# Kernel optimization log

Hardware: AMD Instinct MI355X
Metric: run time of the kernel (lower is better)

The kernel has to match this reference:

```python
import jax, jax.numpy as jnp
import numpy as np

B, T, H, U = 32, 2048, 512, 32

def _glorot(key, shape):
    fan_in, fan_out = shape[0], shape[1]
    limit = np.sqrt(6.0 / (fan_in + fan_out))
    return jax.random.uniform(key, shape, jnp.float32, -limit, limit)

def setup_inputs() -> dict:
    key = jax.random.key(0)
    ks = jax.random.split(key, 6)
    return {
        "x": jax.random.normal(ks[0], (B, T, H), jnp.float32),
        "t": jax.random.normal(ks[1], (B, T, H), jnp.float32),
        "kernel_x": _glorot(ks[2], (H, U)),
        "kernel_t": _glorot(ks[3], (H, U)),
        "kernel_a": _glorot(ks[4], (U, H)),
        "bias_x": jnp.zeros((U,), jnp.float32),
        "bias_t": jnp.zeros((U,), jnp.float32),
        "lambd": _glorot(ks[5], (T, 1)),
    }

def reference(x, t, kernel_x, kernel_t, kernel_a, bias_x, bias_t, lambd):
    # gamma, beta: [B, T, U]
    gamma = jnp.tanh(jnp.einsum('bth,hu->btu', x, kernel_x) + bias_x)
    beta = jnp.tanh(jnp.einsum('bth,hu->btu', t, kernel_t) + bias_t)
    # per-timespan convex combination; lambd [T,1] broadcasts over units
    delta = lambd * gamma + (1.0 - lambd) * beta
    # scores [B, T, H]; softmax over the timespan axis (-2)
    scores = jnp.einsum('btu,uh->bth', delta, kernel_a)
    alpha = jax.nn.softmax(scores, axis=-2)
    return alpha
```

## Files before the change

### kernel.cpp

```cpp
#include <hip/hip_runtime.h>
#include <cmath>

#define Hdim 512
#define Udim 32
#define Bdim 32
#define Tdim 2048
#define RM   64
#define KC   32
#define LDX  36
#define NU   8
#define CH   128

__global__ __launch_bounds__(256, 4) void k1_gemm_act(
    const float* __restrict__ x, const float* __restrict__ tin,
    const float* __restrict__ kx, const float* __restrict__ kt,
    const float* __restrict__ bx, const float* __restrict__ bt,
    const float* __restrict__ lambd, float* __restrict__ delta)
{
    __shared__ float xs[RM * LDX];
    __shared__ float ts[RM * LDX];

    const int tid  = threadIdx.x;
    const int lane = tid & 63;
    const int u0   = __builtin_amdgcn_readfirstlane((tid >> 6) * NU);
    const int row0 = blockIdx.x * RM;

    const int srow = tid >> 3;
    const int sf4  = tid & 7;

    const float4* xg = (const float4*)x;
    const float4* tg = (const float4*)tin;

    float4 px[2], pt[2];
    float accx[NU], acct[NU];
#pragma unroll
    for (int uu = 0; uu < NU; ++uu) { accx[uu] = 0.f; acct[uu] = 0.f; }

#pragma unroll
    for (int l = 0; l < 2; ++l) {
        const size_t r = (size_t)(row0 + srow + 32 * l);
        px[l] = xg[r * (Hdim / 4) + sf4];
        pt[l] = tg[r * (Hdim / 4) + sf4];
    }

#pragma unroll 1
    for (int c = 0; c < Hdim / KC; ++c) {
        __syncthreads();
#pragma unroll
        for (int l = 0; l < 2; ++l) {
            *(float4*)&xs[(srow + 32 * l) * LDX + sf4 * 4] = px[l];
            *(float4*)&ts[(srow + 32 * l) * LDX + sf4 * 4] = pt[l];
        }
        __syncthreads();

        if (c + 1 < Hdim / KC) {
#pragma unroll
            for (int l = 0; l < 2; ++l) {
                const size_t r = (size_t)(row0 + srow + 32 * l);
                px[l] = xg[r * (Hdim / 4) + (c + 1) * (KC / 4) + sf4];
                pt[l] = tg[r * (Hdim / 4) + (c + 1) * (KC / 4) + sf4];
            }
        }

#pragma unroll
        for (int q = 0; q < KC / 4; ++q) {
            float4 av = *(const float4*)&xs[lane * LDX + 4 * q];
            float4 bv = *(const float4*)&ts[lane * LDX + 4 * q];
            float a4[4] = { av.x, av.y, av.z, av.w };
            float b4[4] = { bv.x, bv.y, bv.z, bv.w };
            const float* wxp = kx + (size_t)(c * KC + 4 * q) * Udim + u0;
            const float* wtp = kt + (size_t)(c * KC + 4 * q) * Udim + u0;
#pragma unroll
            for (int kk = 0; kk < 4; ++kk)
#pragma unroll
                for (int uu = 0; uu < NU; ++uu) {
                    accx[uu] = fmaf(a4[kk], wxp[kk * Udim + uu], accx[uu]);
                    acct[uu] = fmaf(b4[kk], wtp[kk * Udim + uu], acct[uu]);
                }
        }
    }

    const int grow = row0 + lane;
    const float lam = lambd[grow & (Tdim - 1)];
    float o[NU];
#pragma unroll
    for (int uu = 0; uu < NU; ++uu) {
        float g  = tanhf(accx[uu] + bx[u0 + uu]);
        float be = tanhf(acct[uu] + bt[u0 + uu]);
        o[uu] = lam * g + (1.0f - lam) * be;
    }
    float* dp = delta + (size_t)grow * Udim + u0;
    *(float4*)&dp[0] = make_float4(o[0], o[1], o[2], o[3]);
    *(float4*)&dp[4] = make_float4(o[4], o[5], o[6], o[7]);
}

__global__ __launch_bounds__(1024, 2) void k2_softmax(
    const float* __restrict__ delta, const float* __restrict__ ka_g,
    float* __restrict__ alpha)
{
    __shared__ float dsm[2][CH * Udim];
    __shared__ float ms[16][64];
    __shared__ float ls[16][64];

    const int tid = threadIdx.x;
    const int tx  = tid & 63;
    const int ty  = tid >> 6;
    const int b   = blockIdx.x & 31;
    const int ht  = blockIdx.x >> 5;
    const int h   = ht * 64 + tx;

    float ka[Udim];
#pragma unroll
    for (int u = 0; u < Udim; ++u) ka[u] = ka_g[u * Hdim + h];

    const float4* dsrc = (const float4*)(delta + (size_t)b * Tdim * Udim);

    ((float4*)dsm[0])[tid] = dsrc[tid];

    float m = -1e30f, l = 0.f;
#pragma unroll 1
    for (int c = 0; c < Tdim / CH; ++c) {
        __syncthreads();
        const float* cur = dsm[c & 1];
        if (c + 1 < Tdim / CH)
            ((float4*)dsm[(c + 1) & 1])[tid] = dsrc[(size_t)(c + 1) * (CH * Udim / 4) + tid];
#pragma unroll
        for (int i = 0; i < CH / 16; ++i) {
            const int r = ty + 16 * i;
            const float4* dp = (const float4*)(cur + r * Udim);
            float4 q[8];
#pragma unroll
            for (int j = 0; j < 8; ++j) q[j] = dp[j];
            float s0 = 0.f, s1 = 0.f, s2 = 0.f, s3 = 0.f;
#pragma unroll
            for (int j = 0; j < 8; ++j) {
                s0 = fmaf(q[j].x, ka[4 * j],     s0);
                s1 = fmaf(q[j].y, ka[4 * j + 1], s1);
                s2 = fmaf(q[j].z, ka[4 * j + 2], s2);
                s3 = fmaf(q[j].w, ka[4 * j + 3], s3);
            }
            const float s = (s0 + s1) + (s2 + s3);
            const float mn = fmaxf(m, s);
            l = l * __expf(m - mn) + __expf(s - mn);
            m = mn;
        }
    }

    ms[ty][tx] = m;
    ls[ty][tx] = l;
    __syncthreads();
    float M = -1e30f;
#pragma unroll
    for (int w = 0; w < 16; ++w) M = fmaxf(M, ms[w][tx]);
    float L = 0.f;
#pragma unroll
    for (int w = 0; w < 16; ++w) L += ls[w][tx] * __expf(ms[w][tx] - M);
    const float rinv = 1.0f / L;

    ((float4*)dsm[0])[tid] = dsrc[tid];

    float* abase = alpha + (size_t)b * Tdim * Hdim + h;
#pragma unroll 1
    for (int c = 0; c < Tdim / CH; ++c) {
        __syncthreads();
        const float* cur = dsm[c & 1];
        if (c + 1 < Tdim / CH)
            ((float4*)dsm[(c + 1) & 1])[tid] = dsrc[(size_t)(c + 1) * (CH * Udim / 4) + tid];
#pragma unroll
        for (int i = 0; i < CH / 16; ++i) {
            const int r = ty + 16 * i;
            const int t = c * CH + r;
            const float4* dp = (const float4*)(cur + r * Udim);
            float4 q[8];
#pragma unroll
            for (int j = 0; j < 8; ++j) q[j] = dp[j];
            float s0 = 0.f, s1 = 0.f, s2 = 0.f, s3 = 0.f;
#pragma unroll
            for (int j = 0; j < 8; ++j) {
                s0 = fmaf(q[j].x, ka[4 * j],     s0);
                s1 = fmaf(q[j].y, ka[4 * j + 1], s1);
                s2 = fmaf(q[j].z, ka[4 * j + 2], s2);
                s3 = fmaf(q[j].w, ka[4 * j + 3], s3);
            }
            const float s = (s0 + s1) + (s2 + s3);
            abase[(size_t)t * Hdim] = __expf(s - M) * rinv;
        }
    }
}

extern "C" void kernel_launch(void* const* d_in, const int* in_sizes, int n_in,
                              void* d_out, int out_size, void* d_ws, size_t ws_size,
                              hipStream_t stream) {
    const float* x     = (const float*)d_in[0];
    const float* tin   = (const float*)d_in[1];
    const float* kx    = (const float*)d_in[2];
    const float* kt    = (const float*)d_in[3];
    const float* ka    = (const float*)d_in[4];
    const float* bx    = (const float*)d_in[5];
    const float* bt    = (const float*)d_in[6];
    const float* lambd = (const float*)d_in[7];
    float* alpha = (float*)d_out;
    float* delta = (float*)d_ws;

    k1_gemm_act<<<(Bdim * Tdim) / RM, 256, 0, stream>>>(x, tin, kx, kt, bx, bt, lambd, delta);
    k2_softmax<<<256, 1024, 0, stream>>>(delta, ka, alpha);
}
```

Baseline: 523.3 us.

## Use split-bf16 MFMA for the input projection GEMM in k1

Replaces the scalar FMA projection in the first kernel with MFMA 16x16x32 bf16 instructions. Activations and weights are split into high and low bf16 parts, and three MFMAs per product recover close to fp32 accuracy. Operands are staged in LDS in an MFMA-friendly layout, with weight tiles now loaded and converted per chunk. This is meant to cut the VALU cost of k1, at the price of conversion work, more LDS traffic and slightly lower precision than true fp32.

Result: faster. 435.2 us (-16.8%).

```diff
diff --git a/kernel.cpp b/kernel.cpp
--- a/kernel.cpp
+++ b/kernel.cpp
@@ -7,9 +7,19 @@
 #define Tdim 2048
 #define RM   64
 #define KC   32
-#define LDX  36
-#define NU   8
 #define CH   128
+
+typedef __attribute__((ext_vector_type(8))) short bf16x8;
+typedef __attribute__((ext_vector_type(4))) float f32x4;
+
+__device__ __forceinline__ unsigned short f2bf(float f) {
+    unsigned int u = __float_as_uint(f);
+    u += 0x7FFFu + ((u >> 16) & 1u);
+    return (unsigned short)(u >> 16);
+}
+__device__ __forceinline__ float bf2f(unsigned short h) {
+    return __uint_as_float(((unsigned int)h) << 16);
+}
 
 __global__ __launch_bounds__(256, 4) void k1_gemm_act(
     const float* __restrict__ x, const float* __restrict__ tin,
@@ -17,81 +27,134 @@
     const float* __restrict__ bx, const float* __restrict__ bt,
     const float* __restrict__ lambd, float* __restrict__ delta)
 {
-    __shared__ float xs[RM * LDX];
-    __shared__ float ts[RM * LDX];
+    __shared__ short axh[2048], axl[2048], ath[2048], atl[2048];
+    __shared__ short wxh[1024], wxl[1024], wth[1024], wtl[1024];
 
     const int tid  = threadIdx.x;
     const int lane = tid & 63;
-    const int u0   = __builtin_amdgcn_readfirstlane((tid >> 6) * NU);
+    const int wv   = tid >> 6;
     const int row0 = blockIdx.x * RM;
 
     const int srow = tid >> 3;
-    const int sf4  = tid & 7;
+    const int sk4  = tid & 7;
+    const int aw_j0    = (sk4 & 1) * 4;
+    const int aw_klane = 16 * (sk4 >> 1);
+    const int su  = tid & 31;
+    const int skq = tid >> 5;
+    const int ww_idx = (su >> 4) * 512 + ((su & 15) + 16 * (skq >> 1)) * 8 + (skq & 1) * 4;
 
     const float4* xg = (const float4*)x;
     const float4* tg = (const float4*)tin;
 
     float4 px[2], pt[2];
-    float accx[NU], acct[NU];
-#pragma unroll
-    for (int uu = 0; uu < NU; ++uu) { accx[uu] = 0.f; acct[uu] = 0.f; }
+    float  pwx[4], pwt[4];
+
+    f32x4 accx[2], acct_[2];
+#pragma unroll
+    for (int ut = 0; ut < 2; ++ut) {
+        accx[ut]  = (f32x4){0.f, 0.f, 0.f, 0.f};
+        acct_[ut] = (f32x4){0.f, 0.f, 0.f, 0.f};
+    }
 
 #pragma unroll
     for (int l = 0; l < 2; ++l) {
-        const size_t r = (size_t)(row0 + srow + 32 * l);
-        px[l] = xg[r * (Hdim / 4) + sf4];
-        pt[l] = tg[r * (Hdim / 4) + sf4];
+        const size_t row = (size_t)(row0 + srow + 32 * l);
+        px[l] = xg[row * (Hdim / 4) + sk4];
+        pt[l] = tg[row * (Hdim / 4) + sk4];
+    }
+#pragma unroll
+    for (int i = 0; i < 4; ++i) {
+        pwx[i] = kx[(size_t)(skq * 4 + i) * Udim + su];
+        pwt[i] = kt[(size_t)(skq * 4 + i) * Udim + su];
     }
 
 #pragma unroll 1
     for (int c = 0; c < Hdim / KC; ++c) {
         __syncthreads();
+
 #pragma unroll
         for (int l = 0; l < 2; ++l) {
-            *(float4*)&xs[(srow + 32 * l) * LDX + sf4 * 4] = px[l];
-            *(float4*)&ts[(srow + 32 * l) * LDX + sf4 * 4] = pt[l];
-        }
-        __syncthreads();
+            const int r   = srow + 32 * l;
+            const int idx = (r >> 4) * 512 + ((r & 15) + aw_klane) * 8 + aw_j0;
+            float4 v = px[l];
+            unsigned short h0 = f2bf(v.x), h1 = f2bf(v.y), h2 = f2bf(v.z), h3 = f2bf(v.w);
+            *(short4*)&axh[idx] = make_short4((short)h0, (short)h1, (short)h2, (short)h3);
+            *(short4*)&axl[idx] = make_short4(
+                (short)f2bf(v.x - bf2f(h0)), (short)f2bf(v.y - bf2f(h1)),
+                (short)f2bf(v.z - bf2f(h2)), (short)f2bf(v.w - bf2f(h3)));
+            v = pt[l];
+            h0 = f2bf(v.x); h1 = f2bf(v.y); h2 = f2bf(v.z); h3 = f2bf(v.w);
+            *(short4*)&ath[idx] = make_short4((short)h0, (short)h1, (short)h2, (short)h3);
+            *(short4*)&atl[idx] = make_short4(
+                (short)f2bf(v.x - bf2f(h0)), (short)f2bf(v.y - bf2f(h1)),
+                (short)f2bf(v.z - bf2f(h2)), (short)f2bf(v.w - bf2f(h3)));
+        }
+        {
+            unsigned short h0 = f2bf(pwx[0]), h1 = f2bf(pwx[1]), h2 = f2bf(pwx[2]), h3 = f2bf(pwx[3]);
+            *(short4*)&wxh[ww_idx] = make_short4((short)h0, (short)h1, (short)h2, (short)h3);
+            *(short4*)&wxl[ww_idx] = make_short4(
+                (short)f2bf(pwx[0] - bf2f(h0)), (short)f2bf(pwx[1] - bf2f(h1)),
+                (short)f2bf(pwx[2] - bf2f(h2)), (short)f2bf(pwx[3] - bf2f(h3)));
+            h0 = f2bf(pwt[0]); h1 = f2bf(pwt[1]); h2 = f2bf(pwt[2]); h3 = f2bf(pwt[3]);
+            *(short4*)&wth[ww_idx] = make_short4((short)h0, (short)h1, (short)h2, (short)h3);
+            *(short4*)&wtl[ww_idx] = make_short4(
+                (short)f2bf(pwt[0] - bf2f(h0)), (short)f2bf(pwt[1] - bf2f(h1)),
+                (short)f2bf(pwt[2] - bf2f(h2)), (short)f2bf(pwt[3] - bf2f(h3)));
+        }
 
         if (c + 1 < Hdim / KC) {
+            const int cn = c + 1;
 #pragma unroll
             for (int l = 0; l < 2; ++l) {
-                const size_t r = (size_t)(row0 + srow + 32 * l);
-                px[l] = xg[r * (Hdim / 4) + (c + 1) * (KC / 4) + sf4];
-                pt[l] = tg[r * (Hdim / 4) + (c + 1) * (KC / 4) + sf4];
-            }
-        }
-
-#pragma unroll
-        for (int q = 0; q < KC / 4; ++q) {
-            float4 av = *(const float4*)&xs[lane * LDX + 4 * q];
-            float4 bv = *(const float4*)&ts[lane * LDX + 4 * q];
-            float a4[4] = { av.x, av.y, av.z, av.w };
-            float b4[4] = { bv.x, bv.y, bv.z, bv.w };
-            const float* wxp = kx + (size_t)(c * KC + 4 * q) * Udim + u0;
-            const float* wtp = kt + (size_t)(c * KC + 4 * q) * Udim + u0;
-#pragma unroll
-            for (int kk = 0; kk < 4; ++kk)
-#pragma unroll
-                for (int uu = 0; uu < NU; ++uu) {
-                    accx[uu] = fmaf(a4[kk], wxp[kk * Udim + uu], accx[uu]);
-                    acct[uu] = fmaf(b4[kk], wtp[kk * Udim + uu], acct[uu]);
-                }
-        }
-    }
-
-    const int grow = row0 + lane;
-    const float lam = lambd[grow & (Tdim - 1)];
-    float o[NU];
-#pragma unroll
-    for (int uu = 0; uu < NU; ++uu) {
-        float g  = tanhf(accx[uu] + bx[u0 + uu]);
-        float be = tanhf(acct[uu] + bt[u0 + uu]);
-        o[uu] = lam * g + (1.0f - lam) * be;
-    }
-    float* dp = delta + (size_t)grow * Udim + u0;
-    *(float4*)&dp[0] = make_float4(o[0], o[1], o[2], o[3]);
-    *(float4*)&dp[4] = make_float4(o[4], o[5], o[6], o[7]);
+                const size_t row = (size_t)(row0 + srow + 32 * l);
+                px[l] = xg[row * (Hdim / 4) + cn * (KC / 4) + sk4];
+                pt[l] = tg[row * (Hdim / 4) + cn * (KC / 4) + sk4];
+            }
+#pragma unroll
+            for (int i = 0; i < 4; ++i) {
+                pwx[i] = kx[(size_t)(cn * KC + skq * 4 + i) * Udim + su];
+                pwt[i] = kt[(size_t)(cn * KC + skq * 4 + i) * Udim + su];
+            }
+        }
+
+        __syncthreads();
+
+        const int ab = wv * 512 + lane * 8;
+        bf16x8 Axh = *(const bf16x8*)&axh[ab];
+        bf16x8 Axl = *(const bf16x8*)&axl[ab];
+        bf16x8 Ath = *(const bf16x8*)&ath[ab];
+        bf16x8 Atl = *(const bf16x8*)&atl[ab];
+#pragma unroll
+        for (int ut = 0; ut < 2; ++ut) {
+            const int wb = ut * 512 + lane * 8;
+            bf16x8 Bh = *(const bf16x8*)&wxh[wb];
+            bf16x8 Bl = *(const bf16x8*)&wxl[wb];
+            accx[ut] = __builtin_amdgcn_mfma_f32_16x16x32_bf16(Axh, Bh, accx[ut], 0, 0, 0);
+            accx[ut] = __builtin_amdgcn_mfma_f32_16x16x32_bf16(Axh, Bl, accx[ut], 0, 0, 0);
+            accx[ut] = __builtin_amdgcn_mfma_f32_16x16x32_bf16(Axl, Bh, accx[ut], 0, 0, 0);
+            Bh = *(const bf16x8*)&wth[wb];
+            Bl = *(const bf16x8*)&wtl[wb];
+            acct_[ut] = __builtin_amdgcn_mfma_f32_16x16x32_bf16(Ath, Bh, acct_[ut], 0, 0, 0);
+            acct_[ut] = __builtin_amdgcn_mfma_f32_16x16x32_bf16(Ath, Bl, acct_[ut], 0, 0, 0);
+            acct_[ut] = __builtin_amdgcn_mfma_f32_16x16x32_bf16(Atl, Bh, acct_[ut], 0, 0, 0);
+        }
+    }
+
+    const int crow = (lane >> 4) * 4;
+    const int ccol = lane & 15;
+    const float bx0 = bx[ccol],      bt0 = bt[ccol];
+    const float bx1 = bx[16 + ccol], bt1 = bt[16 + ccol];
+#pragma unroll
+    for (int r = 0; r < 4; ++r) {
+        const int grow = row0 + wv * 16 + crow + r;
+        const float lam = lambd[grow & (Tdim - 1)];
+        float g0  = tanhf(accx[0][r] + bx0);
+        float be0 = tanhf(acct_[0][r] + bt0);
+        float g1  = tanhf(accx[1][r] + bx1);
+        float be1 = tanhf(acct_[1][r] + bt1);
+        delta[(size_t)grow * Udim + ccol]      = lam * g0 + (1.0f - lam) * be0;
+        delta[(size_t)grow * Udim + 16 + ccol] = lam * g1 + (1.0f - lam) * be1;
+    }
 }
 
 __global__ __launch_bounds__(1024, 2) void k2_softmax(
```
